# Performance work log

Hardware: AMD Instinct MI355X
Metric: run time of the kernel (lower is better)

Reference implementation:

```python
import jax, jax.numpy as jnp
import numpy as np

B, H, W, DIM = 8, 32, 32, 768
NUM_HEADS = 12
HEAD_DIM = DIM // NUM_HEADS  # 64
SCALE = HEAD_DIM ** (-0.5)


def setup_inputs() -> dict:
    key = jax.random.key(0)
    ks = jax.random.split(key, 7)
    return {
        "x": jax.random.normal(ks[0], (B, H, W, DIM), dtype=jnp.float32),
        "qkv_w": jax.random.normal(ks[1], (DIM, 3 * DIM), dtype=jnp.float32) * 0.02,
        "qkv_b": jax.random.normal(ks[2], (3 * DIM,), dtype=jnp.float32) * 0.02,
        "proj_w": jax.random.normal(ks[3], (DIM, DIM), dtype=jnp.float32) * 0.02,
        "proj_b": jax.random.normal(ks[4], (DIM,), dtype=jnp.float32) * 0.02,
        "rel_pos_h": jax.random.normal(ks[5], (2 * H - 1, HEAD_DIM), dtype=jnp.float32) * 0.02,
        "rel_pos_w": jax.random.normal(ks[6], (2 * W - 1, HEAD_DIM), dtype=jnp.float32) * 0.02,
    }


def _get_rel_pos(q_size, k_size, rel_pos):
    # q_size == k_size here, so no interpolation branch; coords in [0, 2*size-2]
    coords = jnp.arange(q_size)[:, None] - jnp.arange(k_size)[None, :] + (k_size - 1)
    return rel_pos[coords]  # [q_size, k_size, head_dim]


def reference(x, qkv_w, qkv_b, proj_w, proj_b, rel_pos_h, rel_pos_w):
    b, h, w, dim = x.shape
    n = h * w
    qkv = x.reshape(b, n, dim) @ qkv_w + qkv_b                      # [B, N, 3*dim]
    qkv = qkv.reshape(b, n, 3, NUM_HEADS, HEAD_DIM)
    qkv = jnp.transpose(qkv, (2, 0, 3, 1, 4)).reshape(3, b * NUM_HEADS, n, HEAD_DIM)
    q, k, v = qkv[0], qkv[1], qkv[2]                                # [B*nh, N, hd]

    attn = jnp.einsum("bqc,bkc->bqk", q * SCALE, k)                 # [B*nh, N, N]

    Rh = _get_rel_pos(h, h, rel_pos_h)                              # [H, H, hd]
    Rw = _get_rel_pos(w, w, rel_pos_w)                              # [W, W, hd]
    r_q = q.reshape(b * NUM_HEADS, h, w, HEAD_DIM)
    rel_h = jnp.einsum("bhwc,hkc->bhwk", r_q, Rh)                   # [B*nh, H, W, H]
    rel_w = jnp.einsum("bhwc,wkc->bhwk", r_q, Rw)                   # [B*nh, H, W, W]
    attn = (attn.reshape(b * NUM_HEADS, h, w, h, w)
            + rel_h[:, :, :, :, None]
            + rel_w[:, :, :, None, :]).reshape(b * NUM_HEADS, n, n)

    attn = jax.nn.softmax(attn, axis=-1)
    out = jnp.einsum("bqk,bkc->bqc", attn, v)                       # [B*nh, N, hd]
    out = out.reshape(b, NUM_HEADS, h, w, HEAD_DIM)
    out = jnp.transpose(out, (0, 2, 3, 1, 4)).reshape(b, h, w, dim)
    return out @ proj_w + proj_b
```

## Files before the change

### kernel.cpp

```cpp
#include <hip/hip_runtime.h>


typedef __bf16 bf16;
typedef __bf16 bf16x8 __attribute__((ext_vector_type(8)));
typedef __bf16 bf16x4 __attribute__((ext_vector_type(4)));
typedef float f32x4 __attribute__((ext_vector_type(4)));

#define MFMA16(a, b, c) __builtin_amdgcn_mfma_f32_16x16x32_bf16((a), (b), (c), 0, 0, 0)

__device__ __forceinline__ void gld_lds16(const void* g, void* l) {
  __builtin_amdgcn_global_load_lds(
      (const __attribute__((address_space(1))) void*)g,
      (__attribute__((address_space(3))) void*)l, 16, 0, 0);
}

__global__ __launch_bounds__(256) void cvt_bf16_k(const float* __restrict__ in,
                                                  bf16* __restrict__ out, int n8) {
  int i = blockIdx.x * 256 + threadIdx.x;
  if (i >= n8) return;
  float4 a = ((const float4*)in)[i * 2];
  float4 b = ((const float4*)in)[i * 2 + 1];
  bf16x8 v;
  v[0] = (bf16)a.x; v[1] = (bf16)a.y; v[2] = (bf16)a.z; v[3] = (bf16)a.w;
  v[4] = (bf16)b.x; v[5] = (bf16)b.y; v[6] = (bf16)b.z; v[7] = (bf16)b.w;
  *(bf16x8*)(out + (size_t)i * 8) = v;
}

__global__ __launch_bounds__(256) void cvt_relp_k(const float* __restrict__ rh,
                                                  const float* __restrict__ rw,
                                                  bf16* __restrict__ rhb,
                                                  bf16* __restrict__ rwb) {
  int idx = blockIdx.x * 256 + threadIdx.x;
  int tab = idx >= 5120;
  int local = idx - (tab ? 5120 : 0);
  int r = local >> 6, c = local & 63;
  const float* src = tab ? rw : rh;
  bf16* dst = tab ? rwb : rhb;
  dst[r * 64 + c] = (bf16)((r < 63) ? src[r * 64 + c] : 0.f);
}

__global__ __launch_bounds__(256) void tconv_k(const float* __restrict__ in,
                                               bf16* __restrict__ out, int K, int N) {
  __shared__ float tile[64][65];
  int k0 = blockIdx.x * 64, n0 = blockIdx.y * 64;
  int tid = threadIdx.x;
#pragma unroll
  for (int it = 0; it < 4; ++it) {
    int f4 = it * 256 + tid;
    int row = f4 >> 4, c4 = f4 & 15;
    float4 v = *(const float4*)(in + (size_t)(k0 + row) * N + n0 + c4 * 4);
    tile[row][c4 * 4 + 0] = v.x; tile[row][c4 * 4 + 1] = v.y;
    tile[row][c4 * 4 + 2] = v.z; tile[row][c4 * 4 + 3] = v.w;
  }
  __syncthreads();
#pragma unroll
  for (int it = 0; it < 2; ++it) {
    int f8 = it * 256 + tid;
    int nrow = f8 >> 3, kc = (f8 & 7) * 8;
    bf16x8 v;
#pragma unroll
    for (int i = 0; i < 8; ++i) v[i] = (bf16)tile[kc + i][nrow];
    *(bf16x8*)(out + (size_t)(n0 + nrow) * K + k0 + kc) = v;
  }
}

template <int MODE>
__global__ __launch_bounds__(256) void gemm_bt_k(const bf16* __restrict__ A,
                                                 const bf16* __restrict__ Bt,
                                                 const float* __restrict__ bias,
                                                 void* __restrict__ outp,
                                                 bf16* __restrict__ vt,
                                                 int M, int N, int K) {
  __shared__ bf16 lA[128 * 32];
  __shared__ bf16 lB[128 * 32];
  int tid = threadIdx.x;
  int wid = tid >> 6, lane = tid & 63;
  int lr = lane & 15, lg = lane >> 4;
  int m0 = blockIdx.x * 128, n0 = blockIdx.y * 128;
  int wr = (wid >> 1) * 64, wc = (wid & 1) * 64;

  const f32x4 fz = {0.f, 0.f, 0.f, 0.f};
  f32x4 acc[4][4];
#pragma unroll
  for (int i = 0; i < 4; ++i)
#pragma unroll
    for (int j = 0; j < 4; ++j) acc[i][j] = fz;

  for (int k0 = 0; k0 < K; k0 += 32) {
    __syncthreads();
#pragma unroll
    for (int it = 0; it < 2; ++it) {
      int e = it * 2048 + tid * 8;
      int row = e >> 5, col = e & 31;
      gld_lds16(A + (size_t)(m0 + row) * K + k0 + col, &lA[it * 2048 + wid * 512]);
      gld_lds16(Bt + (size_t)(n0 + row) * K + k0 + col, &lB[it * 2048 + wid * 512]);
    }
    __syncthreads();
    bf16x8 af[4], bfr[4];
#pragma unroll
    for (int i = 0; i < 4; ++i) {
      af[i]  = *(const bf16x8*)(&lA[(wr + i * 16 + lr) * 32 + lg * 8]);
      bfr[i] = *(const bf16x8*)(&lB[(wc + i * 16 + lr) * 32 + lg * 8]);
    }
#pragma unroll
    for (int mi = 0; mi < 4; ++mi)
#pragma unroll
      for (int ni = 0; ni < 4; ++ni)
        acc[mi][ni] = MFMA16(af[mi], bfr[ni], acc[mi][ni]);
  }

  if (MODE == 0) {
    bf16* qkv = (bf16*)outp;
#pragma unroll
    for (int ni = 0; ni < 4; ++ni) {
      int j = n0 + wc + ni * 16 + lr;
      int three = j / 768;
      int rem = j - three * 768;
      int head = rem >> 6, c = rem & 63;
      float bv = bias[j];
#pragma unroll
      for (int mi = 0; mi < 4; ++mi) {
        int mrow = m0 + wr + mi * 16 + lg * 4;
        int b_ = mrow >> 10, n = mrow & 1023;
        if (three == 2) {
          bf16x4 w4;
#pragma unroll
          for (int r = 0; r < 4; ++r) w4[r] = (bf16)(acc[mi][ni][r] + bv);
          *(bf16x4*)(vt + ((size_t)(b_ * 12 + head) << 16) + (size_t)c * 1024 + n) = w4;
        } else {
          bf16* p = qkv + (size_t)three * 6291456 +
                    ((size_t)(b_ * 12 + head) << 16) + ((size_t)n << 6) + c;
#pragma unroll
          for (int r = 0; r < 4; ++r)
            p[(size_t)r << 6] = (bf16)(acc[mi][ni][r] + bv);
        }
      }
    }
  } else {
    float* Co = (float*)outp;
#pragma unroll
    for (int ni = 0; ni < 4; ++ni) {
      int j = n0 + wc + ni * 16 + lr;
      float bv = bias[j];
#pragma unroll
      for (int mi = 0; mi < 4; ++mi) {
        int mrow = m0 + wr + mi * 16 + lg * 4;
        float* p = Co + (size_t)mrow * N + j;
#pragma unroll
        for (int r = 0; r < 4; ++r)
          p[(size_t)r * N] = acc[mi][ni][r] + bv;
      }
    }
  }
}

__global__ __launch_bounds__(256) void attn_k(const bf16* __restrict__ Qg,
                                              const bf16* __restrict__ Kg,
                                              const bf16* __restrict__ Vg,
                                              const bf16* __restrict__ RHb,
                                              const bf16* __restrict__ RWb,
                                              bf16* __restrict__ attout) {
  __shared__ __align__(16) char smem[40448];
  bf16* lK    = (bf16*)smem;
  bf16* lV    = (bf16*)(smem + 9216);
  bf16* relhd = (bf16*)(smem + 18432);
  unsigned int* lPw = (unsigned int*)(smem + 31232);

  int bh = blockIdx.x, qt = blockIdx.y;
  int bb = bh / 12, head = bh - bb * 12;
  int tid = threadIdx.x, wid = tid >> 6, lane = tid & 63;
  int lr = lane & 15, lg = lane >> 4;
  const size_t bhoff = (size_t)bh << 16;
  const f32x4 fz = {0.f, 0.f, 0.f, 0.f};
  const float LOG2E = 1.44269504f;

  bf16x8 qa[2][2];
#pragma unroll
  for (int f = 0; f < 2; ++f)
#pragma unroll
    for (int h = 0; h < 2; ++h)
      qa[f][h] = *(const bf16x8*)(Qg + bhoff +
                   (size_t)(qt * 128 + wid * 32 + f * 16 + lr) * 64 + h * 32 + lg * 8);

  bf16* scr = (bf16*)(smem + wid * 4352);
#pragma unroll
  for (int f = 0; f < 2; ++f)
#pragma unroll
    for (int tt = 0; tt < 4; ++tt) {
      bf16x8 w0 = *(const bf16x8*)(RWb + (tt * 16 + lr) * 64 + lg * 8);
      bf16x8 w1 = *(const bf16x8*)(RWb + (tt * 16 + lr) * 64 + 32 + lg * 8);
      f32x4 dw = MFMA16(w0, qa[f][0], fz);
      dw = MFMA16(w1, qa[f][1], dw);
#pragma unroll
      for (int r = 0; r < 4; ++r)
        scr[(f * 16 + lr) * 68 + tt * 16 + lg * 4 + r] = (bf16)dw[r];
    }
  float rws[2][8];
#pragma unroll
  for (int f = 0; f < 2; ++f)
#pragma unroll
    for (int tb = 0; tb < 2; ++tb)
#pragma unroll
      for (int r = 0; r < 4; ++r) {
        int kd = (f * 16 + lr) - (tb * 16 + lg * 4 + r) + 31;
        rws[f][tb * 4 + r] = LOG2E * (float)scr[(f * 16 + lr) * 68 + kd];
      }

#pragma unroll
  for (int f = 0; f < 2; ++f)
#pragma unroll
    for (int tt = 0; tt < 3; ++tt) {
      bf16x8 h0 = *(const bf16x8*)(RHb + (4 * qt + tt * 16 + lr) * 64 + lg * 8);
      bf16x8 h1 = *(const bf16x8*)(RHb + (4 * qt + tt * 16 + lr) * 64 + 32 + lg * 8);
      f32x4 dh = MFMA16(h0, qa[f][0], fz);
      dh = MFMA16(h1, qa[f][1], dh);
#pragma unroll
      for (int r = 0; r < 4; ++r)
        relhd[(wid * 32 + f * 16 + lr) * 50 + tt * 16 + lg * 4 + r] = (bf16)dh[r];
    }

  float mst[2] = {-1e30f, -1e30f}, lst[2] = {0.f, 0.f};
  f32x4 oacc[2][4];
#pragma unroll
  for (int f = 0; f < 2; ++f)
#pragma unroll
    for (int ct = 0; ct < 4; ++ct) oacc[f][ct] = fz;

  unsigned int* lPmy = lPw + wid * 576;

  for (int kb = 0; kb < 16; ++kb) {
    __syncthreads();
    {
      int row = tid >> 3, c0s = (tid & 7) * 8;
#pragma unroll
      for (int it = 0; it < 2; ++it) {
        int rr = row + it * 32;
        *(bf16x8*)(&lK[rr * 72 + c0s]) =
            *(const bf16x8*)(Kg + bhoff + (size_t)(kb * 64 + rr) * 64 + c0s);
        *(bf16x8*)(&lV[rr * 72 + c0s]) =
            *(const bf16x8*)(Vg + bhoff + (size_t)rr * 1024 + kb * 64 + c0s);
      }
    }
    __syncthreads();

#pragma unroll
    for (int f = 0; f < 2; ++f) {
      f32x4 s[4];
#pragma unroll
      for (int t = 0; t < 4; ++t) {
        bf16x8 kf0 = *(const bf16x8*)(&lK[(t * 16 + lr) * 72 + lg * 8]);
        bf16x8 kf1 = *(const bf16x8*)(&lK[(t * 16 + lr) * 72 + 32 + lg * 8]);
        s[t] = MFMA16(kf0, qa[f][0], fz);
        s[t] = MFMA16(kf1, qa[f][1], s[t]);
      }
      int rowb = (wid * 32 + f * 16 + lr) * 50;
      float rh0 = LOG2E * (float)relhd[rowb + wid + 31 - 2 * kb];
      float rh1 = LOG2E * (float)relhd[rowb + wid + 30 - 2 * kb];

      float pm = -1e30f;
#pragma unroll
      for (int t = 0; t < 4; ++t)
#pragma unroll
        for (int r = 0; r < 4; ++r) {
          float v = fmaf(s[t][r], 0.18033688f, (t < 2 ? rh0 : rh1) + rws[f][(t & 1) * 4 + r]);
          s[t][r] = v;
          pm = fmaxf(pm, v);
        }
      pm = fmaxf(pm, __shfl_xor(pm, 16));
      pm = fmaxf(pm, __shfl_xor(pm, 32));

      float mnew = fmaxf(mst[f], pm);
      float al = exp2f(mst[f] - mnew);
      mst[f] = mnew;
      float rs = 0.f;
#pragma unroll
      for (int t = 0; t < 4; ++t)
#pragma unroll
        for (int r = 0; r < 4; ++r) {
          float p = exp2f(s[t][r] - mnew);
          s[t][r] = p;
          rs += p;
        }
      rs += __shfl_xor(rs, 16);
      rs += __shfl_xor(rs, 32);
      lst[f] = lst[f] * al + rs;
#pragma unroll
      for (int ct = 0; ct < 4; ++ct)
#pragma unroll
        for (int r = 0; r < 4; ++r) oacc[f][ct][r] *= al;

#pragma unroll
      for (int t = 0; t < 4; ++t)
#pragma unroll
        for (int h = 0; h < 2; ++h) {
          unsigned int u0 = __builtin_bit_cast(unsigned short, (bf16)s[t][2 * h]);
          unsigned int u1 = __builtin_bit_cast(unsigned short, (bf16)s[t][2 * h + 1]);
          lPmy[lr * 36 + t * 8 + lg * 2 + h] = u0 | (u1 << 16);
        }
#pragma unroll
      for (int kk = 0; kk < 2; ++kk) {
        bf16x8 pf = *(const bf16x8*)(&lPmy[lr * 36 + kk * 16 + lg * 4]);
#pragma unroll
        for (int ct = 0; ct < 4; ++ct) {
          bf16x8 vf = *(const bf16x8*)(&lV[(ct * 16 + lr) * 72 + kk * 32 + lg * 8]);
          oacc[f][ct] = MFMA16(vf, pf, oacc[f][ct]);
        }
      }
    }
  }

#pragma unroll
  for (int f = 0; f < 2; ++f) {
    float rl = 1.f / lst[f];
    int n = qt * 128 + wid * 32 + f * 16 + lr;
#pragma unroll
    for (int ct = 0; ct < 4; ++ct) {
      bf16x4 w4;
#pragma unroll
      for (int r = 0; r < 4; ++r) w4[r] = (bf16)(oacc[f][ct][r] * rl);
      *(bf16x4*)(attout + (size_t)(bb * 1024 + n) * 768 + head * 64 + ct * 16 + lg * 4) = w4;
    }
  }
}

extern "C" void kernel_launch(void* const* d_in, const int* in_sizes, int n_in,
                              void* d_out, int out_size, void* d_ws, size_t ws_size,
                              hipStream_t stream) {
  const float* x      = (const float*)d_in[0];
  const float* qkv_w  = (const float*)d_in[1];
  const float* qkv_b  = (const float*)d_in[2];
  const float* proj_w = (const float*)d_in[3];
  const float* proj_b = (const float*)d_in[4];
  const float* relph  = (const float*)d_in[5];
  const float* relpw  = (const float*)d_in[6];
  float* out = (float*)d_out;

  char* ws = (char*)d_ws;
  size_t off = 0;
  auto alloc = [&](size_t bytes) -> void* {
    void* p = ws + off;
    off += (bytes + 255) & ~(size_t)255;
    return p;
  };
  bf16* xb     = (bf16*)alloc(8192UL * 768 * 2);
  bf16* WqkvT  = (bf16*)alloc(2304UL * 768 * 2);
  bf16* WprojT = (bf16*)alloc(768UL * 768 * 2);
  bf16* QKVb   = (bf16*)alloc(2UL * 96 * 1024 * 64 * 2);
  bf16* VTb    = (bf16*)alloc(96UL * 64 * 1024 * 2);
  bf16* RHb    = (bf16*)alloc(80UL * 64 * 2);
  bf16* RWb    = (bf16*)alloc(80UL * 64 * 2);
  bf16* attb   = xb;

  cvt_bf16_k<<<dim3(3072), dim3(256), 0, stream>>>(x, xb, 786432);
  cvt_relp_k<<<dim3(40), dim3(256), 0, stream>>>(relph, relpw, RHb, RWb);
  tconv_k<<<dim3(12, 36), dim3(256), 0, stream>>>(qkv_w, WqkvT, 768, 2304);
  tconv_k<<<dim3(12, 12), dim3(256), 0, stream>>>(proj_w, WprojT, 768, 768);
  gemm_bt_k<0><<<dim3(64, 18), dim3(256), 0, stream>>>(xb, WqkvT, qkv_b,
                                                       (void*)QKVb, VTb, 8192, 2304, 768);
  attn_k<<<dim3(96, 8), dim3(256), 0, stream>>>(QKVb, QKVb + 6291456, VTb,
                                                RHb, RWb, attb);
  gemm_bt_k<1><<<dim3(64, 6), dim3(256), 0, stream>>>(attb, WprojT, proj_b,
                                                      (void*)out, nullptr, 8192, 768, 768);
}
```

Before: 243.1 us.

## Fuse prep kernels and double-buffer K/V with lazy rescaling in attention

Merges the four preprocessing launches (x cast, rel-pos cast, two weight transposes) into one kernel to cut launch overhead. The attention kernel now prefetches the next K/V tile into registers and double-buffers it in LDS, which removes one barrier per iteration. It also skips the online-softmax rescale unless the running max grows by more than 8, computes the row sum with an MFMA against a ones vector instead of shuffles, and raises wave priority around the MFMA sections. These changes trade more LDS per block (which may lower occupancy) for less synchronization and less VALU work.

Result: no change. 239.4 us (-1.5%).

```diff
diff --git a/kernel.cpp b/kernel.cpp
--- a/kernel.cpp
+++ b/kernel.cpp
@@ -4,6 +4,7 @@
 typedef __bf16 bf16;
 typedef __bf16 bf16x8 __attribute__((ext_vector_type(8)));
 typedef __bf16 bf16x4 __attribute__((ext_vector_type(4)));
+typedef __bf16 bf16x2 __attribute__((ext_vector_type(2)));
 typedef float f32x4 __attribute__((ext_vector_type(4)));
 
 #define MFMA16(a, b, c) __builtin_amdgcn_mfma_f32_16x16x32_bf16((a), (b), (c), 0, 0, 0)
@@ -14,36 +15,41 @@
       (__attribute__((address_space(3))) void*)l, 16, 0, 0);
 }
 
-__global__ __launch_bounds__(256) void cvt_bf16_k(const float* __restrict__ in,
-                                                  bf16* __restrict__ out, int n8) {
-  int i = blockIdx.x * 256 + threadIdx.x;
-  if (i >= n8) return;
-  float4 a = ((const float4*)in)[i * 2];
-  float4 b = ((const float4*)in)[i * 2 + 1];
-  bf16x8 v;
-  v[0] = (bf16)a.x; v[1] = (bf16)a.y; v[2] = (bf16)a.z; v[3] = (bf16)a.w;
-  v[4] = (bf16)b.x; v[5] = (bf16)b.y; v[6] = (bf16)b.z; v[7] = (bf16)b.w;
-  *(bf16x8*)(out + (size_t)i * 8) = v;
-}
-
-__global__ __launch_bounds__(256) void cvt_relp_k(const float* __restrict__ rh,
-                                                  const float* __restrict__ rw,
-                                                  bf16* __restrict__ rhb,
-                                                  bf16* __restrict__ rwb) {
-  int idx = blockIdx.x * 256 + threadIdx.x;
-  int tab = idx >= 5120;
-  int local = idx - (tab ? 5120 : 0);
-  int r = local >> 6, c = local & 63;
-  const float* src = tab ? rw : rh;
-  bf16* dst = tab ? rwb : rhb;
-  dst[r * 64 + c] = (bf16)((r < 63) ? src[r * 64 + c] : 0.f);
-}
-
-__global__ __launch_bounds__(256) void tconv_k(const float* __restrict__ in,
-                                               bf16* __restrict__ out, int K, int N) {
+__global__ __launch_bounds__(256) void prep_k(const float* __restrict__ x,
+                                              const float* __restrict__ qkv_w,
+                                              const float* __restrict__ proj_w,
+                                              const float* __restrict__ rh,
+                                              const float* __restrict__ rw,
+                                              bf16* __restrict__ xb,
+                                              bf16* __restrict__ WqkvT,
+                                              bf16* __restrict__ WprojT,
+                                              bf16* __restrict__ rhb,
+                                              bf16* __restrict__ rwb) {
   __shared__ float tile[64][65];
-  int k0 = blockIdx.x * 64, n0 = blockIdx.y * 64;
-  int tid = threadIdx.x;
+  int b = blockIdx.x, tid = threadIdx.x;
+  if (b >= 616) {
+    int i = (b - 616) * 256 + tid;
+    float4 a = ((const float4*)x)[i * 2];
+    float4 c = ((const float4*)x)[i * 2 + 1];
+    bf16x8 v;
+    v[0] = (bf16)a.x; v[1] = (bf16)a.y; v[2] = (bf16)a.z; v[3] = (bf16)a.w;
+    v[4] = (bf16)c.x; v[5] = (bf16)c.y; v[6] = (bf16)c.z; v[7] = (bf16)c.w;
+    *(bf16x8*)(xb + (size_t)i * 8) = v;
+    return;
+  }
+  if (b >= 576) {
+    int idx = (b - 576) * 256 + tid;
+    int tab = idx >= 5120;
+    int local = idx - (tab ? 5120 : 0);
+    int r = local >> 6, c = local & 63;
+    const float* src = tab ? rw : rh;
+    bf16* dst = tab ? rwb : rhb;
+    dst[r * 64 + c] = (bf16)((r < 63) ? src[r * 64 + c] : 0.f);
+    return;
+  }
+  const float* in; bf16* out; int N, k0, n0;
+  if (b < 432) { in = qkv_w; out = WqkvT; N = 2304; k0 = (b % 12) * 64; n0 = (b / 12) * 64; }
+  else { int bb = b - 432; in = proj_w; out = WprojT; N = 768; k0 = (bb % 12) * 64; n0 = (bb / 12) * 64; }
 #pragma unroll
   for (int it = 0; it < 4; ++it) {
     int f4 = it * 256 + tid;
@@ -60,7 +66,7 @@
     bf16x8 v;
 #pragma unroll
     for (int i = 0; i < 8; ++i) v[i] = (bf16)tile[kc + i][nrow];
-    *(bf16x8*)(out + (size_t)(n0 + nrow) * K + k0 + kc) = v;
+    *(bf16x8*)(out + (size_t)(n0 + nrow) * 768 + k0 + kc) = v;
   }
 }
 
@@ -160,11 +166,9 @@
                                               const bf16* __restrict__ RHb,
                                               const bf16* __restrict__ RWb,
                                               bf16* __restrict__ attout) {
-  __shared__ __align__(16) char smem[40448];
-  bf16* lK    = (bf16*)smem;
-  bf16* lV    = (bf16*)(smem + 9216);
-  bf16* relhd = (bf16*)(smem + 18432);
-  unsigned int* lPw = (unsigned int*)(smem + 31232);
+  __shared__ __align__(16) char smem[59136];
+  bf16* relhd = (bf16*)(smem + 36864);
+  unsigned int* lPw = (unsigned int*)(smem + 49664);
 
   int bh = blockIdx.x, qt = blockIdx.y;
   int bb = bh / 12, head = bh - bb * 12;
@@ -174,6 +178,15 @@
   const f32x4 fz = {0.f, 0.f, 0.f, 0.f};
   const float LOG2E = 1.44269504f;
 
+  int srow = tid >> 3, scol = (tid & 7) * 8;
+  const bf16* Ksrc = Kg + bhoff + (size_t)srow * 64 + scol;
+  const bf16* Vsrc = Vg + bhoff + (size_t)srow * 1024 + scol;
+
+  bf16x8 kr0 = *(const bf16x8*)(Ksrc);
+  bf16x8 kr1 = *(const bf16x8*)(Ksrc + 32 * 64);
+  bf16x8 vr0 = *(const bf16x8*)(Vsrc);
+  bf16x8 vr1 = *(const bf16x8*)(Vsrc + 32 * 1024);
+
   bf16x8 qa[2][2];
 #pragma unroll
   for (int f = 0; f < 2; ++f)
@@ -218,34 +231,43 @@
       for (int r = 0; r < 4; ++r)
         relhd[(wid * 32 + f * 16 + lr) * 50 + tt * 16 + lg * 4 + r] = (bf16)dh[r];
     }
-
-  float mst[2] = {-1e30f, -1e30f}, lst[2] = {0.f, 0.f};
-  f32x4 oacc[2][4];
-#pragma unroll
-  for (int f = 0; f < 2; ++f)
+  __syncthreads();
+
+  float mst[2] = {-1e30f, -1e30f};
+  f32x4 oacc[2][4], accl[2];
+  bf16x8 ones;
+#pragma unroll
+  for (int i = 0; i < 8; ++i) ones[i] = (bf16)1.0f;
+#pragma unroll
+  for (int f = 0; f < 2; ++f) {
+    accl[f] = fz;
 #pragma unroll
     for (int ct = 0; ct < 4; ++ct) oacc[f][ct] = fz;
+  }
 
   unsigned int* lPmy = lPw + wid * 576;
 
   for (int kb = 0; kb < 16; ++kb) {
-    __syncthreads();
-    {
-      int row = tid >> 3, c0s = (tid & 7) * 8;
-#pragma unroll
-      for (int it = 0; it < 2; ++it) {
-        int rr = row + it * 32;
-        *(bf16x8*)(&lK[rr * 72 + c0s]) =
-            *(const bf16x8*)(Kg + bhoff + (size_t)(kb * 64 + rr) * 64 + c0s);
-        *(bf16x8*)(&lV[rr * 72 + c0s]) =
-            *(const bf16x8*)(Vg + bhoff + (size_t)rr * 1024 + kb * 64 + c0s);
-      }
+    bf16* lK = (bf16*)(smem + (kb & 1) * 18432);
+    bf16* lV = (bf16*)(smem + (kb & 1) * 18432 + 9216);
+    *(bf16x8*)(&lK[srow * 72 + scol]) = kr0;
+    *(bf16x8*)(&lK[(srow + 32) * 72 + scol]) = kr1;
+    *(bf16x8*)(&lV[srow * 72 + scol]) = vr0;
+    *(bf16x8*)(&lV[(srow + 32) * 72 + scol]) = vr1;
+    if (kb < 15) {
+      const bf16* kp = Ksrc + (kb + 1) * 4096;
+      const bf16* vp = Vsrc + (kb + 1) * 64;
+      kr0 = *(const bf16x8*)(kp);
+      kr1 = *(const bf16x8*)(kp + 32 * 64);
+      vr0 = *(const bf16x8*)(vp);
+      vr1 = *(const bf16x8*)(vp + 32 * 1024);
     }
     __syncthreads();
 
 #pragma unroll
     for (int f = 0; f < 2; ++f) {
       f32x4 s[4];
+      __builtin_amdgcn_s_setprio(1);
 #pragma unroll
       for (int t = 0; t < 4; ++t) {
         bf16x8 kf0 = *(const bf16x8*)(&lK[(t * 16 + lr) * 72 + lg * 8]);
@@ -253,65 +275,64 @@
         s[t] = MFMA16(kf0, qa[f][0], fz);
         s[t] = MFMA16(kf1, qa[f][1], s[t]);
       }
+      __builtin_amdgcn_s_setprio(0);
       int rowb = (wid * 32 + f * 16 + lr) * 50;
       float rh0 = LOG2E * (float)relhd[rowb + wid + 31 - 2 * kb];
       float rh1 = LOG2E * (float)relhd[rowb + wid + 30 - 2 * kb];
 
+#pragma unroll
+      for (int t = 0; t < 4; ++t)
+#pragma unroll
+        for (int r = 0; r < 4; ++r)
+          s[t][r] = fmaf(s[t][r], 0.18033688f,
+                         (t < 2 ? rh0 : rh1) + rws[f][(t & 1) * 4 + r]);
       float pm = -1e30f;
 #pragma unroll
       for (int t = 0; t < 4; ++t)
-#pragma unroll
-        for (int r = 0; r < 4; ++r) {
-          float v = fmaf(s[t][r], 0.18033688f, (t < 2 ? rh0 : rh1) + rws[f][(t & 1) * 4 + r]);
-          s[t][r] = v;
-          pm = fmaxf(pm, v);
-        }
+        pm = fmaxf(pm, fmaxf(fmaxf(s[t][0], s[t][1]), fmaxf(s[t][2], s[t][3])));
       pm = fmaxf(pm, __shfl_xor(pm, 16));
       pm = fmaxf(pm, __shfl_xor(pm, 32));
 
-      float mnew = fmaxf(mst[f], pm);
-      float al = exp2f(mst[f] - mnew);
-      mst[f] = mnew;
-      float rs = 0.f;
+      if (__any((int)(pm - mst[f] > 8.f))) {
+        float mnew = fmaxf(mst[f], pm);
+        float al = exp2f(mst[f] - mnew);
+        mst[f] = mnew;
+        accl[f] *= al;
+#pragma unroll
+        for (int ct = 0; ct < 4; ++ct)
+#pragma unroll
+          for (int r = 0; r < 4; ++r) oacc[f][ct][r] *= al;
+      }
 #pragma unroll
       for (int t = 0; t < 4; ++t)
 #pragma unroll
-        for (int r = 0; r < 4; ++r) {
-          float p = exp2f(s[t][r] - mnew);
-          s[t][r] = p;
-          rs += p;
+        for (int r = 0; r < 4; ++r) s[t][r] = exp2f(s[t][r] - mst[f]);
+
+#pragma unroll
+      for (int t = 0; t < 4; ++t)
+#pragma unroll
+        for (int h = 0; h < 2; ++h) {
+          bf16x2 p2 = {(bf16)s[t][2 * h], (bf16)s[t][2 * h + 1]};
+          lPmy[lr * 36 + t * 8 + lg * 2 + h] = __builtin_bit_cast(unsigned int, p2);
         }
-      rs += __shfl_xor(rs, 16);
-      rs += __shfl_xor(rs, 32);
-      lst[f] = lst[f] * al + rs;
-#pragma unroll
-      for (int ct = 0; ct < 4; ++ct)
-#pragma unroll
-        for (int r = 0; r < 4; ++r) oacc[f][ct][r] *= al;
-
-#pragma unroll
-      for (int t = 0; t < 4; ++t)
-#pragma unroll
-        for (int h = 0; h < 2; ++h) {
-          unsigned int u0 = __builtin_bit_cast(unsigned short, (bf16)s[t][2 * h]);
-          unsigned int u1 = __builtin_bit_cast(unsigned short, (bf16)s[t][2 * h + 1]);
-          lPmy[lr * 36 + t * 8 + lg * 2 + h] = u0 | (u1 << 16);
-        }
+      __builtin_amdgcn_s_setprio(1);
 #pragma unroll
       for (int kk = 0; kk < 2; ++kk) {
         bf16x8 pf = *(const bf16x8*)(&lPmy[lr * 36 + kk * 16 + lg * 4]);
+        accl[f] = MFMA16(ones, pf, accl[f]);
 #pragma unroll
         for (int ct = 0; ct < 4; ++ct) {
           bf16x8 vf = *(const bf16x8*)(&lV[(ct * 16 + lr) * 72 + kk * 32 + lg * 8]);
           oacc[f][ct] = MFMA16(vf, pf, oacc[f][ct]);
         }
       }
+      __builtin_amdgcn_s_setprio(0);
     }
   }
 
 #pragma unroll
   for (int f = 0; f < 2; ++f) {
-    float rl = 1.f / lst[f];
+    float rl = 1.f / accl[f][0];
     int n = qt * 128 + wid * 32 + f * 16 + lr;
 #pragma unroll
     for (int ct = 0; ct < 4; ++ct) {
@@ -351,10 +372,8 @@
   bf16* RWb    = (bf16*)alloc(80UL * 64 * 2);
   bf16* attb   = xb;
 
-  cvt_bf16_k<<<dim3(3072), dim3(256), 0, stream>>>(x, xb, 786432);
-  cvt_relp_k<<<dim3(40), dim3(256), 0, stream>>>(relph, relpw, RHb, RWb);
-  tconv_k<<<dim3(12, 36), dim3(256), 0, stream>>>(qkv_w, WqkvT, 768, 2304);
-  tconv_k<<<dim3(12, 12), dim3(256), 0, stream>>>(proj_w, WprojT, 768, 768);
+  prep_k<<<dim3(3688), dim3(256), 0, stream>>>(x, qkv_w, proj_w, relph, relpw,
+                                               xb, WqkvT, WprojT, RHb, RWb);
   gemm_bt_k<0><<<dim3(64, 18), dim3(256), 0, stream>>>(xb, WqkvT, qkv_b,
                                                        (void*)QKVb, VTb, 8192, 2304, 768);
   attn_k<<<dim3(96, 8), dim3(256), 0, stream>>>(QKVb, QKVb + 6291456, VTb,
```
